# Performance work log

Measured on AMD Instinct MI355X. Metric: run time of the kernel, lower is better.

## Reference

```python
import jax, jax.numpy as jnp
import numpy as np

N_NODES = 50000
N_EDGES = 640000
N_REL = 200
D_IN = 128
D_OUT = 128


def setup_inputs() -> dict:
    key = jax.random.key(0)
    k1, k2, k3, k4, k5, k6 = jax.random.split(key, 6)
    x = jax.random.normal(k1, (N_NODES, D_IN), dtype=jnp.float32)
    edge_index = jax.random.randint(k2, (2, N_EDGES), 0, N_NODES, dtype=jnp.int64)
    edge_type = jax.random.randint(k3, (N_EDGES,), 0, N_REL, dtype=jnp.int64)
    rel_emb = jax.random.normal(k4, (N_REL, D_IN), dtype=jnp.float32)
    # nn.Linear weights stored as [out_features, in_features]
    W_lin = jax.random.normal(k5, (D_OUT, D_IN), dtype=jnp.float32) * (1.0 / np.sqrt(D_IN))
    # xavier_uniform for attn kernel [1, D_IN]
    limit = np.sqrt(6.0 / (1 + D_IN))
    W_attn = jax.random.uniform(k6, (1, D_IN), dtype=jnp.float32, minval=-limit, maxval=limit)
    return {"x": x, "edge_index": edge_index, "edge_type": edge_type,
            "rel_emb": rel_emb, "W_lin": W_lin, "W_attn": W_attn}


def reference(x, edge_index, edge_type, rel_emb, W_lin, W_attn):
    # x: [N, D_in]; edge_index: [2, E]; edge_type: [E]; rel_emb: [R, D_in]
    x_trans = x @ W_lin.T                       # [N, D_out]
    src_idx, tgt_idx = edge_index[0], edge_index[1]
    h_src = x[src_idx]                          # [E, D_in] gather
    h_rel = rel_emb[edge_type]                  # [E, D_in] gather
    sum_feat = h_src + h_rel                    # [E, D_in]
    attn = jax.nn.sigmoid(sum_feat @ W_attn.T)  # [E, 1]
    msg = x_trans[src_idx] * attn               # [E, D_out]
    out = jax.ops.segment_sum(msg, tgt_idx, num_segments=x.shape[0])  # [N, D_out]
    return jax.nn.relu(out)
```

## Files before the change

### kernel.cpp

```cpp
#include <hip/hip_runtime.h>
#include <hip/hip_bf16.h>

#define N_NODES 50000
#define N_EDGES 640000
#define N_REL   200
#define D       128
#define CAP     64
#define RANGES  8
#define NODES_PER_RANGE (N_NODES / RANGES)
#define CHUNK_EDGES 2560
#define N_CHUNKS (N_EDGES / CHUNK_EDGES)

#define XT_WAVES   (N_NODES / 16)
#define XT_GROUPS  98
#define SC_GROUPS  N_CHUNKS
#define TOT_GROUPS (XT_GROUPS + SC_GROUPS)

typedef __attribute__((ext_vector_type(8))) short short8;
typedef __attribute__((ext_vector_type(4))) float floatx4;
typedef __attribute__((ext_vector_type(4))) unsigned uintx4;

__device__ __forceinline__ unsigned short f2bf(float f) {
    unsigned u = __float_as_uint(f);
    u += 0x7FFF + ((u >> 16) & 1);
    return (unsigned short)(u >> 16);
}

__device__ __forceinline__ float sigmoidf(float x) {
    return 1.f / (1.f + __expf(-x));
}

__global__ __launch_bounds__(256) void setup_kernel(
        const float* __restrict__ W,
        const float* __restrict__ x,
        const float* __restrict__ rel,
        const float* __restrict__ Wattn,
        unsigned short* __restrict__ Wbf,
        float* __restrict__ s_rel,
        float* __restrict__ s_node,
        int* __restrict__ count) {
    const int b = blockIdx.x;
    if (b < 64) {
        const int i = b * 256 + threadIdx.x;
        Wbf[i] = f2bf(W[i]);
    } else if (b < 114) {
        const int wave = (b - 64) * 4 + (threadIdx.x >> 6);
        const int lane = threadIdx.x & 63;
        if (wave < N_REL) {
            const float* __restrict__ row = rel + (size_t)wave * D;
            float a = fmaf(row[lane], Wattn[lane],
                           row[lane + 64] * Wattn[lane + 64]);
#pragma unroll
            for (int off = 32; off; off >>= 1)
                a += __shfl_down(a, off);
            if (lane == 0) s_rel[wave] = a;
        }
    } else if (b < 310) {
        const int i = (b - 114) * 256 + threadIdx.x;
        if (i < N_NODES) count[i] = 0;
    } else {
        const int node = (b - 310) * 8 + (threadIdx.x >> 5);
        const int sub  = threadIdx.x & 31;
        if (node < N_NODES) {
            const float4 xv = ((const float4*)(x + (size_t)node * D))[sub];
            const float4 wv = ((const float4*)Wattn)[sub];
            float a = xv.x * wv.x + xv.y * wv.y + xv.z * wv.z + xv.w * wv.w;
#pragma unroll
            for (int off = 16; off; off >>= 1)
                a += __shfl_xor(a, off);
            if (sub == 0) s_node[node] = a;
        }
    }
}

__global__ __launch_bounds__(256) void fused_kernel(
        const float* __restrict__ x,
        const unsigned short* __restrict__ Wbf,
        unsigned short* __restrict__ xt,
        const int* __restrict__ src_idx,
        const int* __restrict__ tgt_idx,
        const int* __restrict__ etype,
        const float* __restrict__ s_node,
        const float* __restrict__ s_rel,
        int* __restrict__ count,
        unsigned* __restrict__ sorted) {
    const int g    = blockIdx.x >> 3;
    const int sub8 = blockIdx.x & 7;
    const int xg   = (g * XT_GROUPS) / TOT_GROUPS;
    const bool is_x = (((g + 1) * XT_GROUPS) / TOT_GROUPS) > xg;

    if (is_x) {
        const int wid = (xg * 8 + sub8) * 4 + (threadIdx.x >> 6);
        if (wid >= XT_WAVES) return;
        const int lane = threadIdx.x & 63;
        const int r16  = lane & 15;
        const int quad = lane >> 4;
        const int m0   = wid * 16;

        short8 af[4];
#pragma unroll
        for (int s = 0; s < 4; ++s) {
            const int k0 = s * 32 + quad * 8;
            const float* __restrict__ xr = x + (size_t)(m0 + r16) * D + k0;
            const float4 lo = *(const float4*)(xr);
            const float4 hi = *(const float4*)(xr + 4);
            short8 a;
            a[0] = (short)f2bf(lo.x); a[1] = (short)f2bf(lo.y);
            a[2] = (short)f2bf(lo.z); a[3] = (short)f2bf(lo.w);
            a[4] = (short)f2bf(hi.x); a[5] = (short)f2bf(hi.y);
            a[6] = (short)f2bf(hi.z); a[7] = (short)f2bf(hi.w);
            af[s] = a;
        }

#pragma unroll
        for (int t = 0; t < 8; ++t) {
            floatx4 acc = {0.f, 0.f, 0.f, 0.f};
#pragma unroll
            for (int s = 0; s < 4; ++s) {
                const int k0 = s * 32 + quad * 8;
                const short8 bfr = *(const short8*)(Wbf + (size_t)(t * 16 + r16) * D + k0);
                acc = __builtin_amdgcn_mfma_f32_16x16x32_bf16(af[s], bfr, acc, 0, 0, 0);
            }
#pragma unroll
            for (int r = 0; r < 4; ++r) {
                const int orow = m0 + quad * 4 + r;
                xt[(size_t)orow * D + t * 16 + r16] = f2bf(acc[r]);
            }
        }
    } else {
        const int sg   = g - xg;
        const int lo   = sub8 * NODES_PER_RANGE;
        const int hi   = lo + NODES_PER_RANGE;
        const int base = sg * CHUNK_EDGES + threadIdx.x;

#pragma unroll
        for (int it = 0; it < CHUNK_EDGES / 256; ++it) {
            const int e = base + it * 256;
            const int t = __builtin_nontemporal_load(tgt_idx + e);
            if (t >= lo && t < hi) {
                const int s = __builtin_nontemporal_load(src_idx + e);
                const int r = __builtin_nontemporal_load(etype + e);
                const float logit = s_node[s] + s_rel[r];
                const unsigned rec =
                    ((unsigned)f2bf(sigmoidf(logit)) << 16) | (unsigned)s;
                const int k = atomicAdd(&count[t], 1);
                sorted[t * CAP + k] = rec;
            }
        }
    }
}

__device__ __forceinline__ void gproc(unsigned r, const unsigned short* __restrict__ xt,
                                      int sub, floatx4& acc) {
    const unsigned src = r & 0xFFFFu;
    const float a = __uint_as_float(r & 0xFFFF0000u);
    const uint2 p = *(const uint2*)(xt + (size_t)src * D + sub * 4);
    acc[0] = fmaf(a, __uint_as_float(p.x << 16),         acc[0]);
    acc[1] = fmaf(a, __uint_as_float(p.x & 0xFFFF0000u), acc[1]);
    acc[2] = fmaf(a, __uint_as_float(p.y << 16),         acc[2]);
    acc[3] = fmaf(a, __uint_as_float(p.y & 0xFFFF0000u), acc[3]);
}

__global__ __launch_bounds__(256) void gather_kernel(
        const int* __restrict__ count,
        const unsigned* __restrict__ sorted,
        const unsigned short* __restrict__ xt,
        float* __restrict__ out) {
    const int wid  = (blockIdx.x * blockDim.x + threadIdx.x) >> 6;
    const int lane = threadIdx.x & 63;
    const int half = lane >> 5;
    const int sub  = lane & 31;
    const int t    = wid * 2 + half;
    if (t >= N_NODES) return;

    const int cnt = count[t];
    const unsigned* __restrict__ rec = sorted + (size_t)t * CAP;

    floatx4 acc = {0.f, 0.f, 0.f, 0.f};
    int i = 0;
    for (; i + 4 <= cnt; i += 4) {
        const uintx4 r4 = __builtin_nontemporal_load((const uintx4*)(rec + i));
        gproc(r4.x, xt, sub, acc);
        gproc(r4.y, xt, sub, acc);
        gproc(r4.z, xt, sub, acc);
        gproc(r4.w, xt, sub, acc);
    }
    for (; i < cnt; ++i)
        gproc(__builtin_nontemporal_load(rec + i), xt, sub, acc);

    floatx4 o;
    o[0] = fmaxf(acc[0], 0.f);
    o[1] = fmaxf(acc[1], 0.f);
    o[2] = fmaxf(acc[2], 0.f);
    o[3] = fmaxf(acc[3], 0.f);
    __builtin_nontemporal_store(o, (floatx4*)(out + (size_t)t * D) + sub);
}

extern "C" void kernel_launch(void* const* d_in, const int* in_sizes, int n_in,
                              void* d_out, int out_size, void* d_ws, size_t ws_size,
                              hipStream_t stream) {
    const float* x        = (const float*)d_in[0];
    const int*   edge_idx = (const int*)d_in[1];
    const int*   etype    = (const int*)d_in[2];
    const float* rel_emb  = (const float*)d_in[3];
    const float* W_lin    = (const float*)d_in[4];
    const float* W_attn   = (const float*)d_in[5];
    float* out = (float*)d_out;

    const int* src_idx = edge_idx;
    const int* tgt_idx = edge_idx + N_EDGES;

    unsigned short* xt   = (unsigned short*)d_ws;
    float* s_node        = (float*)(xt + (size_t)N_NODES * D);
    float* s_rel         = s_node + N_NODES;
    unsigned short* Wbf  = (unsigned short*)(s_rel + N_REL);
    int*   count         = (int*)(Wbf + D * D);
    unsigned* sorted     = (unsigned*)(count + N_NODES);

    setup_kernel<<<dim3(310 + (N_NODES + 7) / 8), dim3(256), 0, stream>>>(
        W_lin, x, rel_emb, W_attn, Wbf, s_rel, s_node, count);

    fused_kernel<<<dim3(TOT_GROUPS * 8), dim3(256), 0, stream>>>(
        x, Wbf, xt, src_idx, tgt_idx, etype, s_node, s_rel, count, sorted);

    gather_kernel<<<dim3(N_NODES / 8), dim3(256), 0, stream>>>(
        count, sorted, xt, out);
}
```

Before: 178.9 us.

## Fold node attention dot into MFMA transform and split scatter into own kernel

The per-node attention logit (x·W_attn) is now computed inside the MFMA transform kernel from the x values it already loads, so the separate pass over x in the setup kernel goes away. The interleaved transform/scatter kernel is split into two sequential launches. The scatter kernel stages s_rel in shared memory and loads all three edge index arrays unconditionally with ordinary loads instead of nontemporal ones. This removes one full read of x but adds a kernel launch and gives up the overlap between the GEMM and the scatter work.

```diff
diff --git a/kernel.cpp b/kernel.cpp
--- a/kernel.cpp
+++ b/kernel.cpp
@@ -11,11 +11,6 @@
 #define CHUNK_EDGES 2560
 #define N_CHUNKS (N_EDGES / CHUNK_EDGES)
 
-#define XT_WAVES   (N_NODES / 16)
-#define XT_GROUPS  98
-#define SC_GROUPS  N_CHUNKS
-#define TOT_GROUPS (XT_GROUPS + SC_GROUPS)
-
 typedef __attribute__((ext_vector_type(8))) short short8;
 typedef __attribute__((ext_vector_type(4))) float floatx4;
 typedef __attribute__((ext_vector_type(4))) unsigned uintx4;
@@ -32,12 +27,10 @@
 
 __global__ __launch_bounds__(256) void setup_kernel(
         const float* __restrict__ W,
-        const float* __restrict__ x,
         const float* __restrict__ rel,
         const float* __restrict__ Wattn,
         unsigned short* __restrict__ Wbf,
         float* __restrict__ s_rel,
-        float* __restrict__ s_node,
         int* __restrict__ count) {
     const int b = blockIdx.x;
     if (b < 64) {
@@ -55,28 +48,68 @@
                 a += __shfl_down(a, off);
             if (lane == 0) s_rel[wave] = a;
         }
-    } else if (b < 310) {
+    } else {
         const int i = (b - 114) * 256 + threadIdx.x;
         if (i < N_NODES) count[i] = 0;
-    } else {
-        const int node = (b - 310) * 8 + (threadIdx.x >> 5);
-        const int sub  = threadIdx.x & 31;
-        if (node < N_NODES) {
-            const float4 xv = ((const float4*)(x + (size_t)node * D))[sub];
-            const float4 wv = ((const float4*)Wattn)[sub];
-            float a = xv.x * wv.x + xv.y * wv.y + xv.z * wv.z + xv.w * wv.w;
-#pragma unroll
-            for (int off = 16; off; off >>= 1)
-                a += __shfl_xor(a, off);
-            if (sub == 0) s_node[node] = a;
-        }
-    }
-}
-
-__global__ __launch_bounds__(256) void fused_kernel(
+    }
+}
+
+__global__ __launch_bounds__(256) void xtrans_mfma_kernel(
         const float* __restrict__ x,
         const unsigned short* __restrict__ Wbf,
+        const float* __restrict__ Wattn,
         unsigned short* __restrict__ xt,
+        float* __restrict__ s_node) {
+    const int wid = (blockIdx.x * blockDim.x + threadIdx.x) >> 6;
+    if (wid >= N_NODES / 16) return;
+    const int lane = threadIdx.x & 63;
+    const int r16  = lane & 15;
+    const int quad = lane >> 4;
+    const int m0   = wid * 16;
+
+    short8 af[4];
+    float  sn = 0.f;
+#pragma unroll
+    for (int s = 0; s < 4; ++s) {
+        const int k0 = s * 32 + quad * 8;
+        const float* __restrict__ xr = x + (size_t)(m0 + r16) * D + k0;
+        const float4 lo = *(const float4*)(xr);
+        const float4 hi = *(const float4*)(xr + 4);
+        const float4 wl = *(const float4*)(Wattn + k0);
+        const float4 wh = *(const float4*)(Wattn + k0 + 4);
+        sn = fmaf(lo.x, wl.x, sn); sn = fmaf(lo.y, wl.y, sn);
+        sn = fmaf(lo.z, wl.z, sn); sn = fmaf(lo.w, wl.w, sn);
+        sn = fmaf(hi.x, wh.x, sn); sn = fmaf(hi.y, wh.y, sn);
+        sn = fmaf(hi.z, wh.z, sn); sn = fmaf(hi.w, wh.w, sn);
+        short8 a;
+        a[0] = (short)f2bf(lo.x); a[1] = (short)f2bf(lo.y);
+        a[2] = (short)f2bf(lo.z); a[3] = (short)f2bf(lo.w);
+        a[4] = (short)f2bf(hi.x); a[5] = (short)f2bf(hi.y);
+        a[6] = (short)f2bf(hi.z); a[7] = (short)f2bf(hi.w);
+        af[s] = a;
+    }
+    sn += __shfl_xor(sn, 16);
+    sn += __shfl_xor(sn, 32);
+    if (lane < 16) s_node[m0 + r16] = sn;
+
+#pragma unroll
+    for (int t = 0; t < 8; ++t) {
+        floatx4 acc = {0.f, 0.f, 0.f, 0.f};
+#pragma unroll
+        for (int s = 0; s < 4; ++s) {
+            const int k0 = s * 32 + quad * 8;
+            const short8 b = *(const short8*)(Wbf + (size_t)(t * 16 + r16) * D + k0);
+            acc = __builtin_amdgcn_mfma_f32_16x16x32_bf16(af[s], b, acc, 0, 0, 0);
+        }
+#pragma unroll
+        for (int r = 0; r < 4; ++r) {
+            const int orow = m0 + quad * 4 + r;
+            xt[(size_t)orow * D + t * 16 + r16] = f2bf(acc[r]);
+        }
+    }
+}
+
+__global__ __launch_bounds__(256) void scatter_kernel(
         const int* __restrict__ src_idx,
         const int* __restrict__ tgt_idx,
         const int* __restrict__ etype,
@@ -84,68 +117,27 @@
         const float* __restrict__ s_rel,
         int* __restrict__ count,
         unsigned* __restrict__ sorted) {
-    const int g    = blockIdx.x >> 3;
-    const int sub8 = blockIdx.x & 7;
-    const int xg   = (g * XT_GROUPS) / TOT_GROUPS;
-    const bool is_x = (((g + 1) * XT_GROUPS) / TOT_GROUPS) > xg;
-
-    if (is_x) {
-        const int wid = (xg * 8 + sub8) * 4 + (threadIdx.x >> 6);
-        if (wid >= XT_WAVES) return;
-        const int lane = threadIdx.x & 63;
-        const int r16  = lane & 15;
-        const int quad = lane >> 4;
-        const int m0   = wid * 16;
-
-        short8 af[4];
-#pragma unroll
-        for (int s = 0; s < 4; ++s) {
-            const int k0 = s * 32 + quad * 8;
-            const float* __restrict__ xr = x + (size_t)(m0 + r16) * D + k0;
-            const float4 lo = *(const float4*)(xr);
-            const float4 hi = *(const float4*)(xr + 4);
-            short8 a;
-            a[0] = (short)f2bf(lo.x); a[1] = (short)f2bf(lo.y);
-            a[2] = (short)f2bf(lo.z); a[3] = (short)f2bf(lo.w);
-            a[4] = (short)f2bf(hi.x); a[5] = (short)f2bf(hi.y);
-            a[6] = (short)f2bf(hi.z); a[7] = (short)f2bf(hi.w);
-            af[s] = a;
-        }
-
-#pragma unroll
-        for (int t = 0; t < 8; ++t) {
-            floatx4 acc = {0.f, 0.f, 0.f, 0.f};
-#pragma unroll
-            for (int s = 0; s < 4; ++s) {
-                const int k0 = s * 32 + quad * 8;
-                const short8 bfr = *(const short8*)(Wbf + (size_t)(t * 16 + r16) * D + k0);
-                acc = __builtin_amdgcn_mfma_f32_16x16x32_bf16(af[s], bfr, acc, 0, 0, 0);
-            }
-#pragma unroll
-            for (int r = 0; r < 4; ++r) {
-                const int orow = m0 + quad * 4 + r;
-                xt[(size_t)orow * D + t * 16 + r16] = f2bf(acc[r]);
-            }
-        }
-    } else {
-        const int sg   = g - xg;
-        const int lo   = sub8 * NODES_PER_RANGE;
-        const int hi   = lo + NODES_PER_RANGE;
-        const int base = sg * CHUNK_EDGES + threadIdx.x;
-
-#pragma unroll
-        for (int it = 0; it < CHUNK_EDGES / 256; ++it) {
-            const int e = base + it * 256;
-            const int t = __builtin_nontemporal_load(tgt_idx + e);
-            if (t >= lo && t < hi) {
-                const int s = __builtin_nontemporal_load(src_idx + e);
-                const int r = __builtin_nontemporal_load(etype + e);
-                const float logit = s_node[s] + s_rel[r];
-                const unsigned rec =
-                    ((unsigned)f2bf(sigmoidf(logit)) << 16) | (unsigned)s;
-                const int k = atomicAdd(&count[t], 1);
-                sorted[t * CAP + k] = rec;
-            }
+    __shared__ float ls_rel[N_REL];
+    if (threadIdx.x < N_REL) ls_rel[threadIdx.x] = s_rel[threadIdx.x];
+    __syncthreads();
+
+    const int b     = blockIdx.x;
+    const int lo    = (b & 7) * NODES_PER_RANGE;
+    const int hi    = lo + NODES_PER_RANGE;
+    const int base  = (b >> 3) * CHUNK_EDGES + threadIdx.x;
+
+#pragma unroll
+    for (int it = 0; it < CHUNK_EDGES / 256; ++it) {
+        const int e = base + it * 256;
+        const int t = tgt_idx[e];
+        const int s = src_idx[e];
+        const int r = etype[e];
+        if (t >= lo && t < hi) {
+            const float logit = s_node[s] + ls_rel[r];
+            const unsigned rec =
+                ((unsigned)f2bf(sigmoidf(logit)) << 16) | (unsigned)s;
+            const int k = atomicAdd(&count[t], 1);
+            sorted[t * CAP + k] = rec;
         }
     }
 }
@@ -217,11 +209,14 @@
     int*   count         = (int*)(Wbf + D * D);
     unsigned* sorted     = (unsigned*)(count + N_NODES);
 
-    setup_kernel<<<dim3(310 + (N_NODES + 7) / 8), dim3(256), 0, stream>>>(
-        W_lin, x, rel_emb, W_attn, Wbf, s_rel, s_node, count);
-
-    fused_kernel<<<dim3(TOT_GROUPS * 8), dim3(256), 0, stream>>>(
-        x, Wbf, xt, src_idx, tgt_idx, etype, s_node, s_rel, count, sorted);
+    setup_kernel<<<dim3(310), dim3(256), 0, stream>>>(
+        W_lin, rel_emb, W_attn, Wbf, s_rel, count);
+
+    xtrans_mfma_kernel<<<dim3((N_NODES / 16 * 64 + 255) / 256), dim3(256), 0, stream>>>(
+        x, Wbf, W_attn, xt, s_node);
+
+    scatter_kernel<<<dim3(N_CHUNKS * RANGES), dim3(256), 0, stream>>>(
+        src_idx, tgt_idx, etype, s_node, s_rel, count, sorted);
 
     gather_kernel<<<dim3(N_NODES / 8), dim3(256), 0, stream>>>(
         count, sorted, xt, out);
```

Result: faster. 168.1 us (-6.0%).
